# Optimization experiments

Measured on AMD Instinct MI355X. Metric: run time of the kernel, lower is better.

The kernel has to match this reference:

```python
import jax, jax.numpy as jnp
import numpy as np

NUM_CITIES = 88
NUM_YEARS = 6
STDDEVE = 0.01
STDDEVG = 0.1
STDDEVW = 0.1
N_ROWS = 200000


def setup_inputs() -> dict:
    key = jax.random.key(0)
    k = jax.random.split(key, 6)
    G = jax.random.normal(k[0], (N_ROWS, NUM_CITIES), dtype=jnp.float32)
    out = jax.random.normal(k[1], (N_ROWS, NUM_YEARS), dtype=jnp.float32)
    U = jax.random.normal(k[2], (N_ROWS, NUM_YEARS), dtype=jnp.float32)
    V = jax.random.normal(k[3], (N_ROWS, NUM_YEARS), dtype=jnp.float32)
    D = jax.random.normal(k[4], (N_ROWS, NUM_CITIES), dtype=jnp.float32)
    w = jax.random.normal(k[5], (N_ROWS, NUM_CITIES), dtype=jnp.float32)
    return {"G": G, "out": out, "U": U, "V": V, "D": D, "w": w}


def reference(G, out, U, V, D, w):
    # sum over first num_years-1 columns of ||U[:,i]-out[:,i]||_2^2 == Frobenius sq norm
    diff = U[:, : NUM_YEARS - 1] - out[:, : NUM_YEARS - 1]
    loss = jnp.sum(diff * diff)
    # sum_i log(||G[:,i]||_1), all 88 column L1 norms in one fused reduction
    lgg = jnp.sum(jnp.log(jnp.sum(jnp.abs(G), axis=0)))
    loss = loss + (STDDEVE ** 2) * lgg
    # ||G - w*D||_F^2 * stddevg^2 / stddeve^2
    r = G - w * D
    loss = loss + jnp.sum(r * r) * (STDDEVG ** 2 / STDDEVE ** 2)
    # ||w^2||_1 * stddeve^2 / stddevw^2
    loss = loss + jnp.sum(w * w) * (STDDEVE ** 2 / STDDEVW ** 2)
    # penalty: sum over negative entries of G, scaled by 100
    loss = loss + jnp.sum(jnp.where(G < 0, G, 0.0) * 100.0)
    return loss
```

## Files before the change

kernel.cpp:

```cpp
#include <hip/hip_runtime.h>
#include <math.h>

#define NUM_CITIES 88
#define NUM_YEARS 6
#define N_ROWS 200000

#define COL4 (NUM_CITIES / 4)
#define TOT4 (N_ROWS * COL4)
#define DIFF2 (N_ROWS * NUM_YEARS / 2)

#define NBLK 1936
#define NTHREADS (NBLK * 256)
#define NPART 92

#define TAIL_CUT (TOT4 - 8 * NTHREADS)

#define WS2_OFF (NBLK * NPART)

typedef float vf4 __attribute__((ext_vector_type(4)));
typedef float vf2 __attribute__((ext_vector_type(2)));

static __device__ __forceinline__ vf4 ldnt4(const float* p) {
    return __builtin_nontemporal_load((const vf4*)p);
}
static __device__ __forceinline__ vf2 ldnt2(const float* p) {
    return __builtin_nontemporal_load((const vf2*)p);
}

__global__ __launch_bounds__(256) void loss_main(
    const float* __restrict__ G,
    const float* __restrict__ outm,
    const float* __restrict__ U,
    const float* __restrict__ D,
    const float* __restrict__ w,
    float* __restrict__ ws)
{
    __shared__ float scol[NUM_CITIES];
    __shared__ float ssum[4];

    const int tid = threadIdx.x;
    const int gtid = blockIdx.x * blockDim.x + tid;
    const int c0 = (gtid % COL4) * 4;

    vf4 g0 = ldnt4(G + 4 * ((size_t)gtid + 0 * NTHREADS));
    vf4 g1 = ldnt4(G + 4 * ((size_t)gtid + 1 * NTHREADS));
    vf4 g2 = ldnt4(G + 4 * ((size_t)gtid + 2 * NTHREADS));
    vf4 g3 = ldnt4(G + 4 * ((size_t)gtid + 3 * NTHREADS));
    vf4 g4 = ldnt4(G + 4 * ((size_t)gtid + 4 * NTHREADS));
    vf4 g5 = ldnt4(G + 4 * ((size_t)gtid + 5 * NTHREADS));
    vf4 g6 = ldnt4(G + 4 * ((size_t)gtid + 6 * NTHREADS));
    vf4 g7 = ldnt4(G + 4 * ((size_t)gtid + 7 * NTHREADS));
    vf4 d0 = ldnt4(D + 4 * ((size_t)gtid + 0 * NTHREADS));
    vf4 d1 = ldnt4(D + 4 * ((size_t)gtid + 1 * NTHREADS));
    vf4 d2 = ldnt4(D + 4 * ((size_t)gtid + 2 * NTHREADS));
    vf4 d3 = ldnt4(D + 4 * ((size_t)gtid + 3 * NTHREADS));
    vf4 d4 = ldnt4(D + 4 * ((size_t)gtid + 4 * NTHREADS));
    vf4 d5 = ldnt4(D + 4 * ((size_t)gtid + 5 * NTHREADS));
    vf4 d6 = ldnt4(D + 4 * ((size_t)gtid + 6 * NTHREADS));
    vf4 d7 = ldnt4(D + 4 * ((size_t)gtid + 7 * NTHREADS));
    vf4 v0 = ldnt4(w + 4 * ((size_t)gtid + 0 * NTHREADS));
    vf4 v1 = ldnt4(w + 4 * ((size_t)gtid + 1 * NTHREADS));
    vf4 v2 = ldnt4(w + 4 * ((size_t)gtid + 2 * NTHREADS));
    vf4 v3 = ldnt4(w + 4 * ((size_t)gtid + 3 * NTHREADS));
    vf4 v4 = ldnt4(w + 4 * ((size_t)gtid + 4 * NTHREADS));
    vf4 v5 = ldnt4(w + 4 * ((size_t)gtid + 5 * NTHREADS));
    vf4 v6 = ldnt4(w + 4 * ((size_t)gtid + 6 * NTHREADS));
    vf4 v7 = ldnt4(w + 4 * ((size_t)gtid + 7 * NTHREADS));

    float ca0 = 0.f, ca1 = 0.f, ca2 = 0.f, ca3 = 0.f;
    float s_r2 = 0.f, s_w2 = 0.f, s_neg = 0.f;

#define ACC(g, d, v)                                                          \
    {                                                                         \
        ca0 += fabsf(g.x); ca1 += fabsf(g.y);                                 \
        ca2 += fabsf(g.z); ca3 += fabsf(g.w);                                 \
        float r0 = g.x - v.x * d.x, r1 = g.y - v.y * d.y;                     \
        float r2 = g.z - v.z * d.z, r3 = g.w - v.w * d.w;                     \
        s_r2 += r0 * r0 + r1 * r1 + r2 * r2 + r3 * r3;                        \
        s_w2 += v.x * v.x + v.y * v.y + v.z * v.z + v.w * v.w;                \
        s_neg += fminf(g.x, 0.f) + fminf(g.y, 0.f)                            \
               + fminf(g.z, 0.f) + fminf(g.w, 0.f);                          \
    }

    ACC(g0, d0, v0) ACC(g1, d1, v1) ACC(g2, d2, v2) ACC(g3, d3, v3)
    ACC(g4, d4, v4) ACC(g5, d5, v5) ACC(g6, d6, v6) ACC(g7, d7, v7)

    if (gtid < TAIL_CUT) {
        vf4 g = ldnt4(G + 4 * ((size_t)gtid + 8 * NTHREADS));
        vf4 d = ldnt4(D + 4 * ((size_t)gtid + 8 * NTHREADS));
        vf4 v = ldnt4(w + 4 * ((size_t)gtid + 8 * NTHREADS));
        ACC(g, d, v)
    }
#undef ACC

    float s_diff = 0.f;
    {
        vf2 u = ldnt2(U + 2 * (size_t)gtid), o = ldnt2(outm + 2 * (size_t)gtid);
        float dx = u.x - o.x, dy = u.y - o.y;
        s_diff += dx * dx + ((gtid % 3 != 2) ? dy * dy : 0.f);
        const int i2 = gtid + NTHREADS;
        if (i2 < DIFF2) {
            vf2 u2 = ldnt2(U + 2 * (size_t)i2), o2 = ldnt2(outm + 2 * (size_t)i2);
            float ex = u2.x - o2.x, ey = u2.y - o2.y;
            s_diff += ex * ex + ((i2 % 3 != 2) ? ey * ey : 0.f);
        }
    }

    if (tid < NUM_CITIES) scol[tid] = 0.f;
    if (tid < 4) ssum[tid] = 0.f;
    __syncthreads();

    atomicAdd(&scol[c0 + 0], ca0);
    atomicAdd(&scol[c0 + 1], ca1);
    atomicAdd(&scol[c0 + 2], ca2);
    atomicAdd(&scol[c0 + 3], ca3);

    for (int off = 32; off > 0; off >>= 1) {
        s_diff += __shfl_down(s_diff, off);
        s_r2   += __shfl_down(s_r2, off);
        s_w2   += __shfl_down(s_w2, off);
        s_neg  += __shfl_down(s_neg, off);
    }
    if ((tid & 63) == 0) {
        atomicAdd(&ssum[0], s_diff);
        atomicAdd(&ssum[1], s_r2);
        atomicAdd(&ssum[2], s_w2);
        atomicAdd(&ssum[3], s_neg);
    }
    __syncthreads();

    float* dst = ws + (size_t)blockIdx.x * NPART;
    if (tid < NUM_CITIES) dst[tid] = scol[tid];
    else if (tid < NPART)  dst[tid] = ssum[tid - NUM_CITIES];
}

__global__ __launch_bounds__(256) void loss_reduce(float* __restrict__ ws)
{
    const int k = blockIdx.x;
    const int t = threadIdx.x;
    float acc = 0.f;
    for (int b = t; b < NBLK; b += 256)
        acc += ws[(size_t)b * NPART + k];
    for (int off = 32; off > 0; off >>= 1) acc += __shfl_down(acc, off);
    __shared__ float s[4];
    if ((t & 63) == 0) s[t >> 6] = acc;
    __syncthreads();
    if (t == 0) ws[WS2_OFF + k] = s[0] + s[1] + s[2] + s[3];
}

__global__ __launch_bounds__(128) void loss_finalize(
    const float* __restrict__ ws, float* __restrict__ out)
{
    __shared__ float sh[2];
    const int t = threadIdx.x;
    const float* ws2 = ws + WS2_OFF;

    float v = 0.f;
    if (t < NUM_CITIES)      v = 1e-4f * logf(ws2[t]);
    else if (t == 88)        v = ws2[88];
    else if (t == 89)        v = 100.f * ws2[89];
    else if (t == 90)        v = 0.01f * ws2[90];
    else if (t == 91)        v = 100.f * ws2[91];

    for (int off = 32; off > 0; off >>= 1) v += __shfl_down(v, off);
    if (t == 0)  sh[0] = v;
    if (t == 64) sh[1] = v;
    __syncthreads();
    if (t == 0) out[0] = sh[0] + sh[1];
}

extern "C" void kernel_launch(void* const* d_in, const int* in_sizes, int n_in,
                              void* d_out, int out_size, void* d_ws, size_t ws_size,
                              hipStream_t stream) {
    const float* G    = (const float*)d_in[0];
    const float* outm = (const float*)d_in[1];
    const float* U    = (const float*)d_in[2];
    const float* D    = (const float*)d_in[4];
    const float* w    = (const float*)d_in[5];
    float* out = (float*)d_out;
    float* ws  = (float*)d_ws;

    loss_main<<<NBLK, 256, 0, stream>>>(G, outm, U, D, w, ws);
    loss_reduce<<<NPART, 256, 0, stream>>>(ws);
    loss_finalize<<<1, 128, 0, stream>>>(ws, out);
}
```

Measured before the change: 208.8 us.

## Fuse reduce and finalize via last-block counter, transpose partials, drop nontemporal loads

The separate finalize kernel is merged into the reduce kernel: each block bumps an atomic counter and the last block to arrive computes the final loss, saving one kernel launch. Per-block partials are now stored transposed, so each reduce block reads a contiguous stripe. Main-kernel input loads switch from nontemporal to ordinary loads. The counter is never reset and relies on modulo NPART across calls, so it assumes the workspace starts zeroed or consistent.

```diff
diff --git a/kernel.cpp b/kernel.cpp
--- a/kernel.cpp
+++ b/kernel.cpp
@@ -15,16 +15,17 @@
 
 #define TAIL_CUT (TOT4 - 8 * NTHREADS)
 
-#define WS2_OFF (NBLK * NPART)
+#define WS2_OFF (NPART * NBLK)
+#define CTR_OFF (WS2_OFF + NPART)
 
 typedef float vf4 __attribute__((ext_vector_type(4)));
 typedef float vf2 __attribute__((ext_vector_type(2)));
 
-static __device__ __forceinline__ vf4 ldnt4(const float* p) {
-    return __builtin_nontemporal_load((const vf4*)p);
+static __device__ __forceinline__ vf4 ld4(const float* p) {
+    return *(const vf4*)p;
 }
-static __device__ __forceinline__ vf2 ldnt2(const float* p) {
-    return __builtin_nontemporal_load((const vf2*)p);
+static __device__ __forceinline__ vf2 ld2(const float* p) {
+    return *(const vf2*)p;
 }
 
 __global__ __launch_bounds__(256) void loss_main(
@@ -42,30 +43,30 @@
     const int gtid = blockIdx.x * blockDim.x + tid;
     const int c0 = (gtid % COL4) * 4;
 
-    vf4 g0 = ldnt4(G + 4 * ((size_t)gtid + 0 * NTHREADS));
-    vf4 g1 = ldnt4(G + 4 * ((size_t)gtid + 1 * NTHREADS));
-    vf4 g2 = ldnt4(G + 4 * ((size_t)gtid + 2 * NTHREADS));
-    vf4 g3 = ldnt4(G + 4 * ((size_t)gtid + 3 * NTHREADS));
-    vf4 g4 = ldnt4(G + 4 * ((size_t)gtid + 4 * NTHREADS));
-    vf4 g5 = ldnt4(G + 4 * ((size_t)gtid + 5 * NTHREADS));
-    vf4 g6 = ldnt4(G + 4 * ((size_t)gtid + 6 * NTHREADS));
-    vf4 g7 = ldnt4(G + 4 * ((size_t)gtid + 7 * NTHREADS));
-    vf4 d0 = ldnt4(D + 4 * ((size_t)gtid + 0 * NTHREADS));
-    vf4 d1 = ldnt4(D + 4 * ((size_t)gtid + 1 * NTHREADS));
-    vf4 d2 = ldnt4(D + 4 * ((size_t)gtid + 2 * NTHREADS));
-    vf4 d3 = ldnt4(D + 4 * ((size_t)gtid + 3 * NTHREADS));
-    vf4 d4 = ldnt4(D + 4 * ((size_t)gtid + 4 * NTHREADS));
-    vf4 d5 = ldnt4(D + 4 * ((size_t)gtid + 5 * NTHREADS));
-    vf4 d6 = ldnt4(D + 4 * ((size_t)gtid + 6 * NTHREADS));
-    vf4 d7 = ldnt4(D + 4 * ((size_t)gtid + 7 * NTHREADS));
-    vf4 v0 = ldnt4(w + 4 * ((size_t)gtid + 0 * NTHREADS));
-    vf4 v1 = ldnt4(w + 4 * ((size_t)gtid + 1 * NTHREADS));
-    vf4 v2 = ldnt4(w + 4 * ((size_t)gtid + 2 * NTHREADS));
-    vf4 v3 = ldnt4(w + 4 * ((size_t)gtid + 3 * NTHREADS));
-    vf4 v4 = ldnt4(w + 4 * ((size_t)gtid + 4 * NTHREADS));
-    vf4 v5 = ldnt4(w + 4 * ((size_t)gtid + 5 * NTHREADS));
-    vf4 v6 = ldnt4(w + 4 * ((size_t)gtid + 6 * NTHREADS));
-    vf4 v7 = ldnt4(w + 4 * ((size_t)gtid + 7 * NTHREADS));
+    vf4 g0 = ld4(G + 4 * ((size_t)gtid + 0 * NTHREADS));
+    vf4 g1 = ld4(G + 4 * ((size_t)gtid + 1 * NTHREADS));
+    vf4 g2 = ld4(G + 4 * ((size_t)gtid + 2 * NTHREADS));
+    vf4 g3 = ld4(G + 4 * ((size_t)gtid + 3 * NTHREADS));
+    vf4 g4 = ld4(G + 4 * ((size_t)gtid + 4 * NTHREADS));
+    vf4 g5 = ld4(G + 4 * ((size_t)gtid + 5 * NTHREADS));
+    vf4 g6 = ld4(G + 4 * ((size_t)gtid + 6 * NTHREADS));
+    vf4 g7 = ld4(G + 4 * ((size_t)gtid + 7 * NTHREADS));
+    vf4 d0 = ld4(D + 4 * ((size_t)gtid + 0 * NTHREADS));
+    vf4 d1 = ld4(D + 4 * ((size_t)gtid + 1 * NTHREADS));
+    vf4 d2 = ld4(D + 4 * ((size_t)gtid + 2 * NTHREADS));
+    vf4 d3 = ld4(D + 4 * ((size_t)gtid + 3 * NTHREADS));
+    vf4 d4 = ld4(D + 4 * ((size_t)gtid + 4 * NTHREADS));
+    vf4 d5 = ld4(D + 4 * ((size_t)gtid + 5 * NTHREADS));
+    vf4 d6 = ld4(D + 4 * ((size_t)gtid + 6 * NTHREADS));
+    vf4 d7 = ld4(D + 4 * ((size_t)gtid + 7 * NTHREADS));
+    vf4 v0 = ld4(w + 4 * ((size_t)gtid + 0 * NTHREADS));
+    vf4 v1 = ld4(w + 4 * ((size_t)gtid + 1 * NTHREADS));
+    vf4 v2 = ld4(w + 4 * ((size_t)gtid + 2 * NTHREADS));
+    vf4 v3 = ld4(w + 4 * ((size_t)gtid + 3 * NTHREADS));
+    vf4 v4 = ld4(w + 4 * ((size_t)gtid + 4 * NTHREADS));
+    vf4 v5 = ld4(w + 4 * ((size_t)gtid + 5 * NTHREADS));
+    vf4 v6 = ld4(w + 4 * ((size_t)gtid + 6 * NTHREADS));
+    vf4 v7 = ld4(w + 4 * ((size_t)gtid + 7 * NTHREADS));
 
     float ca0 = 0.f, ca1 = 0.f, ca2 = 0.f, ca3 = 0.f;
     float s_r2 = 0.f, s_w2 = 0.f, s_neg = 0.f;
@@ -86,21 +87,21 @@
     ACC(g4, d4, v4) ACC(g5, d5, v5) ACC(g6, d6, v6) ACC(g7, d7, v7)
 
     if (gtid < TAIL_CUT) {
-        vf4 g = ldnt4(G + 4 * ((size_t)gtid + 8 * NTHREADS));
-        vf4 d = ldnt4(D + 4 * ((size_t)gtid + 8 * NTHREADS));
-        vf4 v = ldnt4(w + 4 * ((size_t)gtid + 8 * NTHREADS));
+        vf4 g = ld4(G + 4 * ((size_t)gtid + 8 * NTHREADS));
+        vf4 d = ld4(D + 4 * ((size_t)gtid + 8 * NTHREADS));
+        vf4 v = ld4(w + 4 * ((size_t)gtid + 8 * NTHREADS));
         ACC(g, d, v)
     }
 #undef ACC
 
     float s_diff = 0.f;
     {
-        vf2 u = ldnt2(U + 2 * (size_t)gtid), o = ldnt2(outm + 2 * (size_t)gtid);
+        vf2 u = ld2(U + 2 * (size_t)gtid), o = ld2(outm + 2 * (size_t)gtid);
         float dx = u.x - o.x, dy = u.y - o.y;
         s_diff += dx * dx + ((gtid % 3 != 2) ? dy * dy : 0.f);
         const int i2 = gtid + NTHREADS;
         if (i2 < DIFF2) {
-            vf2 u2 = ldnt2(U + 2 * (size_t)i2), o2 = ldnt2(outm + 2 * (size_t)i2);
+            vf2 u2 = ld2(U + 2 * (size_t)i2), o2 = ld2(outm + 2 * (size_t)i2);
             float ex = u2.x - o2.x, ey = u2.y - o2.y;
             s_diff += ex * ex + ((i2 % 3 != 2) ? ey * ey : 0.f);
         }
@@ -129,32 +130,39 @@
     }
     __syncthreads();
 
-    float* dst = ws + (size_t)blockIdx.x * NPART;
-    if (tid < NUM_CITIES) dst[tid] = scol[tid];
-    else if (tid < NPART)  dst[tid] = ssum[tid - NUM_CITIES];
+    if (tid < NUM_CITIES)
+        ws[(size_t)tid * NBLK + blockIdx.x] = scol[tid];
+    else if (tid < NPART)
+        ws[(size_t)tid * NBLK + blockIdx.x] = ssum[tid - NUM_CITIES];
 }
 
-__global__ __launch_bounds__(256) void loss_reduce(float* __restrict__ ws)
+__global__ __launch_bounds__(256) void loss_reduce_fin(
+    float* __restrict__ ws, float* __restrict__ out)
 {
     const int k = blockIdx.x;
     const int t = threadIdx.x;
+
+    const float* src = ws + (size_t)k * NBLK;
     float acc = 0.f;
     for (int b = t; b < NBLK; b += 256)
-        acc += ws[(size_t)b * NPART + k];
+        acc += src[b];
     for (int off = 32; off > 0; off >>= 1) acc += __shfl_down(acc, off);
+
     __shared__ float s[4];
+    __shared__ int last;
     if ((t & 63) == 0) s[t >> 6] = acc;
     __syncthreads();
-    if (t == 0) ws[WS2_OFF + k] = s[0] + s[1] + s[2] + s[3];
-}
+    if (t == 0) {
+        ws[WS2_OFF + k] = s[0] + s[1] + s[2] + s[3];
+        __threadfence();
+        unsigned old = atomicAdd((unsigned int*)(ws + CTR_OFF), 1u);
+        last = ((old % NPART) == (NPART - 1)) ? 1 : 0;
+    }
+    __syncthreads();
+    if (!last) return;
 
-__global__ __launch_bounds__(128) void loss_finalize(
-    const float* __restrict__ ws, float* __restrict__ out)
-{
-    __shared__ float sh[2];
-    const int t = threadIdx.x;
+    __threadfence();
     const float* ws2 = ws + WS2_OFF;
-
     float v = 0.f;
     if (t < NUM_CITIES)      v = 1e-4f * logf(ws2[t]);
     else if (t == 88)        v = ws2[88];
@@ -163,10 +171,10 @@
     else if (t == 91)        v = 100.f * ws2[91];
 
     for (int off = 32; off > 0; off >>= 1) v += __shfl_down(v, off);
-    if (t == 0)  sh[0] = v;
-    if (t == 64) sh[1] = v;
+    __shared__ float sh[4];
+    if ((t & 63) == 0) sh[t >> 6] = v;
     __syncthreads();
-    if (t == 0) out[0] = sh[0] + sh[1];
+    if (t == 0) out[0] = sh[0] + sh[1] + sh[2] + sh[3];
 }
 
 extern "C" void kernel_launch(void* const* d_in, const int* in_sizes, int n_in,
@@ -181,6 +189,5 @@
     float* ws  = (float*)d_ws;
 
     loss_main<<<NBLK, 256, 0, stream>>>(G, outm, U, D, w, ws);
-    loss_reduce<<<NPART, 256, 0, stream>>>(ws);
-    loss_finalize<<<1, 128, 0, stream>>>(ws, out);
+    loss_reduce_fin<<<NPART, 256, 0, stream>>>(ws, out);
 }
```

After: 226.5 us. 8.5% more time.

## Fuse reduce and finalize via last-block counter; transpose partials layout

Applied to the files above, without the earlier changes.

Partial sums are now stored partition-major, so each reduce block reads a contiguous run instead of a strided column. The separate finalize kernel is merged into the reduce kernel: each block bumps a global counter after a threadfence, and the last block to finish computes the final loss. This removes one kernel launch and makes the partial reads coalesced. In exchange it relies on a counter in the workspace that is never reset; using modulo NPART keeps it correct across repeated calls, assuming the workspace starts at zero or a multiple of NPART.

```diff
diff --git a/kernel.cpp b/kernel.cpp
--- a/kernel.cpp
+++ b/kernel.cpp
@@ -15,7 +15,8 @@
 
 #define TAIL_CUT (TOT4 - 8 * NTHREADS)
 
-#define WS2_OFF (NBLK * NPART)
+#define WS2_OFF (NPART * NBLK)
+#define CTR_OFF (WS2_OFF + NPART)
 
 typedef float vf4 __attribute__((ext_vector_type(4)));
 typedef float vf2 __attribute__((ext_vector_type(2)));
@@ -129,32 +130,39 @@
     }
     __syncthreads();
 
-    float* dst = ws + (size_t)blockIdx.x * NPART;
-    if (tid < NUM_CITIES) dst[tid] = scol[tid];
-    else if (tid < NPART)  dst[tid] = ssum[tid - NUM_CITIES];
+    if (tid < NUM_CITIES)
+        ws[(size_t)tid * NBLK + blockIdx.x] = scol[tid];
+    else if (tid < NPART)
+        ws[(size_t)tid * NBLK + blockIdx.x] = ssum[tid - NUM_CITIES];
 }
 
-__global__ __launch_bounds__(256) void loss_reduce(float* __restrict__ ws)
+__global__ __launch_bounds__(256) void loss_reduce_fin(
+    float* __restrict__ ws, float* __restrict__ out)
 {
     const int k = blockIdx.x;
     const int t = threadIdx.x;
+
+    const float* src = ws + (size_t)k * NBLK;
     float acc = 0.f;
     for (int b = t; b < NBLK; b += 256)
-        acc += ws[(size_t)b * NPART + k];
+        acc += src[b];
     for (int off = 32; off > 0; off >>= 1) acc += __shfl_down(acc, off);
+
     __shared__ float s[4];
+    __shared__ int last;
     if ((t & 63) == 0) s[t >> 6] = acc;
     __syncthreads();
-    if (t == 0) ws[WS2_OFF + k] = s[0] + s[1] + s[2] + s[3];
-}
+    if (t == 0) {
+        ws[WS2_OFF + k] = s[0] + s[1] + s[2] + s[3];
+        __threadfence();
+        unsigned old = atomicAdd((unsigned int*)(ws + CTR_OFF), 1u);
+        last = ((old % NPART) == (NPART - 1)) ? 1 : 0;
+    }
+    __syncthreads();
+    if (!last) return;
 
-__global__ __launch_bounds__(128) void loss_finalize(
-    const float* __restrict__ ws, float* __restrict__ out)
-{
-    __shared__ float sh[2];
-    const int t = threadIdx.x;
+    __threadfence();
     const float* ws2 = ws + WS2_OFF;
-
     float v = 0.f;
     if (t < NUM_CITIES)      v = 1e-4f * logf(ws2[t]);
     else if (t == 88)        v = ws2[88];
@@ -163,10 +171,10 @@
     else if (t == 91)        v = 100.f * ws2[91];
 
     for (int off = 32; off > 0; off >>= 1) v += __shfl_down(v, off);
-    if (t == 0)  sh[0] = v;
-    if (t == 64) sh[1] = v;
+    __shared__ float sh[4];
+    if ((t & 63) == 0) sh[t >> 6] = v;
     __syncthreads();
-    if (t == 0) out[0] = sh[0] + sh[1];
+    if (t == 0) out[0] = sh[0] + sh[1] + sh[2] + sh[3];
 }
 
 extern "C" void kernel_launch(void* const* d_in, const int* in_sizes, int n_in,
@@ -181,6 +189,5 @@
     float* ws  = (float*)d_ws;
 
     loss_main<<<NBLK, 256, 0, stream>>>(G, outm, U, D, w, ws);
-    loss_reduce<<<NPART, 256, 0, stream>>>(ws);
-    loss_finalize<<<1, 128, 0, stream>>>(ws, out);
+    loss_reduce_fin<<<NPART, 256, 0, stream>>>(ws, out);
 }
```

Measured after the change: 210.6 us. Within noise of the previous version (+0.8%).
